# Kernel optimization log

Measured on AMD Instinct MI355X. Metric: run time of the kernel, lower is better.

The kernel has to match this reference:

```python
import jax, jax.numpy as jnp
import numpy as np

DIM = 128
HEADS = 4
HEAD_DIM = DIM // HEADS
SCALE = HEAD_DIM ** -0.5


def setup_inputs() -> dict:
    k0 = jax.random.key(0)
    ks = jax.random.split(k0, 20)
    B, N, Hq, Wq_, Hk, Wk_ = 1, 6, 100, 100, 16, 44
    s = 0.02
    return {
        "query": jax.random.normal(ks[0], (B, DIM, Hq, Wq_), jnp.float32),
        "key": jax.random.normal(ks[1], (B, N, DIM, Hk, Wk_), jnp.float32),
        "value": jax.random.normal(ks[2], (B, N, DIM, Hk, Wk_), jnp.float32),
        "depth": jax.random.uniform(ks[3], (B, N, 1, Hk, Wk_), jnp.float32),
        "depth_confidence": jax.random.uniform(ks[4], (B, N, 1, Hk, Wk_), jnp.float32),
        "skip": jax.random.normal(ks[5], (B, DIM, Hq, Wq_), jnp.float32),
        "Wq": jax.random.normal(ks[6], (DIM, DIM), jnp.float32) * s,
        "bq": jnp.zeros((DIM,), jnp.float32),
        "Wk": jax.random.normal(ks[7], (DIM, DIM), jnp.float32) * s,
        "bk": jnp.zeros((DIM,), jnp.float32),
        "Wv": jax.random.normal(ks[8], (DIM, DIM), jnp.float32) * s,
        "bv": jnp.zeros((DIM,), jnp.float32),
        "Wo": jax.random.normal(ks[9], (DIM, DIM), jnp.float32) * s,
        "bo": jnp.zeros((DIM,), jnp.float32),
        "dw1": jax.random.normal(ks[10], (DIM // 4, 1), jnp.float32) * s,  # 1x1 conv: 1 -> dim/4
        "db1": jnp.zeros((DIM // 4,), jnp.float32),
        "dw2": jax.random.normal(ks[11], (HEADS, DIM // 4), jnp.float32) * s,  # 1x1 conv: dim/4 -> heads
        "db2": jnp.zeros((HEADS,), jnp.float32),
    }


def _forward(query, key, value, depth, depth_confidence, skip,
             Wq, bq, Wk, bk, Wv, bv, Wo, bo, dw1, db1, dw2, db2):
    B, dim, Hq, Wq_ = query.shape
    N, Hk, Wk_ = key.shape[1], key.shape[3], key.shape[4]
    Lq, Lk = Hq * Wq_, N * Hk * Wk_

    # b d h w -> b (h w) d
    qf = jnp.transpose(query, (0, 2, 3, 1)).reshape(B, Lq, dim)
    # b n d h w -> b (n h w) d
    kf = jnp.transpose(key, (0, 1, 3, 4, 2)).reshape(B, Lk, dim)
    vf = jnp.transpose(value, (0, 1, 3, 4, 2)).reshape(B, Lk, dim)

    def heads(x, W, b):  # (B,L,dim) -> (B,H,L,hd)
        y = x @ W.T + b
        return jnp.transpose(y.reshape(B, -1, HEADS, HEAD_DIM), (0, 2, 1, 3))

    Q = heads(qf, Wq, bq)
    K = heads(kf, Wk, bk)
    V = heads(vf, Wv, bv)

    attn = jnp.einsum('bhqd,bhkd->bhqk', Q, K) * SCALE  # (B,H,Lq,Lk)

    # depth weighting bias: two 1x1 convs + softmax over heads channel
    d = jnp.transpose(depth, (0, 1, 3, 4, 2))  # (B,N,Hk,Wk,1)
    t = jax.nn.relu(d @ dw1.T + db1)            # (B,N,Hk,Wk,dim/4)
    t = t @ dw2.T + db2                          # (B,N,Hk,Wk,heads)
    dw = jax.nn.softmax(t, axis=-1)
    conf = jnp.transpose(depth_confidence, (0, 1, 3, 4, 2))  # (B,N,Hk,Wk,1)
    cw = conf * dw                               # (B,N,Hk,Wk,heads)
    bias = 0.1 * jnp.transpose(cw, (0, 4, 1, 2, 3)).reshape(B, HEADS, 1, Lk)

    attn = jax.nn.softmax(attn + bias, axis=-1)
    out = jnp.einsum('bhqk,bhkd->bhqd', attn, V)             # (B,H,Lq,hd)
    out = jnp.transpose(out, (0, 2, 1, 3)).reshape(B, Lq, dim)
    out = out @ Wo.T + bo
    out = jnp.transpose(out.reshape(B, Hq, Wq_, dim), (0, 3, 1, 2))
    return out + skip


def reference(query, key, value, depth, depth_confidence, skip,
              Wq, bq, Wk, bk, Wv, bv, Wo, bo, dw1, db1, dw2, db2):
    return _forward(query, key, value, depth, depth_confidence, skip,
                    Wq, bq, Wk, bk, Wv, bv, Wo, bo, dw1, db1, dw2, db2)
```

## Files before the change

### kernel.cpp

```cpp
#include <hip/hip_runtime.h>
#include <stdint.h>

#define LQ 10000
#define LK 4224
#define NQB 313
#define SCALE 0.17677669529663687f
#define LOG2E 1.44269504088896341f
#define SCALE2 (SCALE * LOG2E)

typedef __bf16 bf16x8 __attribute__((ext_vector_type(8)));
typedef __bf16 bf16x4 __attribute__((ext_vector_type(4)));
typedef float  f32x4  __attribute__((ext_vector_type(4)));
typedef unsigned short u16x4 __attribute__((ext_vector_type(4)));

__device__ __forceinline__ unsigned short f2b(float f) {
  union { float f; unsigned u; } v; v.f = f;
  unsigned r = v.u + 0x7fffu + ((v.u >> 16) & 1u);
  return (unsigned short)(r >> 16);
}

__global__ void misc_kernel(
    const float* __restrict__ depth, const float* __restrict__ conf,
    const float* __restrict__ dw1, const float* __restrict__ db1,
    const float* __restrict__ dw2, const float* __restrict__ db2,
    const float* __restrict__ Wq, const float* __restrict__ Wk,
    const float* __restrict__ Wv, const float* __restrict__ Wo,
    float* __restrict__ biasArr,
    unsigned short* __restrict__ Wqb, unsigned short* __restrict__ Wkb,
    unsigned short* __restrict__ Wvb, unsigned short* __restrict__ Wob) {
  int b = blockIdx.x, t = threadIdx.x;
  if (b < 256) {
    int i = b * 256 + t;
    int m = i >> 14, j = i & 16383;
    const float* src = (m == 0) ? Wq : (m == 1) ? Wk : (m == 2) ? Wv : Wo;
    unsigned short* dst = (m == 0) ? Wqb : (m == 1) ? Wkb : (m == 2) ? Wvb : Wob;
    dst[j] = f2b(src[j]);
    return;
  }
  int k = (b - 256) * 256 + t;
  if (k >= LK) return;
  float d = depth[k], c = conf[k];
  float t2[4];
#pragma unroll
  for (int hh = 0; hh < 4; ++hh) t2[hh] = db2[hh];
  for (int cc = 0; cc < 32; ++cc) {
    float t1 = fmaxf(fmaf(d, dw1[cc], db1[cc]), 0.f);
#pragma unroll
    for (int hh = 0; hh < 4; ++hh) t2[hh] = fmaf(t1, dw2[hh * 32 + cc], t2[hh]);
  }
  float mx = fmaxf(fmaxf(t2[0], t2[1]), fmaxf(t2[2], t2[3]));
  float e[4], s = 0.f;
#pragma unroll
  for (int hh = 0; hh < 4; ++hh) { e[hh] = __expf(t2[hh] - mx); s += e[hh]; }
  float f = 0.1f * c / s * LOG2E;
#pragma unroll
  for (int hh = 0; hh < 4; ++hh) biasArr[hh * LK + k] = f * e[hh];
}

__global__ __launch_bounds__(256) void proj_q_kernel(
    const float* __restrict__ X, const unsigned short* __restrict__ Wb,
    const float* __restrict__ bias, unsigned short* __restrict__ Y) {
  __shared__ __align__(16) unsigned short Xb[64][136];
  int t = threadIdx.x;
  int l0 = blockIdx.x * 64;
#pragma unroll
  for (int i = 0; i < 32; ++i) {
    int e = t + 256 * i;
    int d = e >> 6, c = e & 63;
    int l = l0 + c;
    Xb[c][d] = f2b(l < LQ ? X[(size_t)d * LQ + l] : 0.f);
  }
  __syncthreads();
  int wv = t >> 6, lane = t & 63, lm = lane & 15, lg = lane >> 4;
  const f32x4 zf = {0.f, 0.f, 0.f, 0.f};
  bf16x8 af[4];
#pragma unroll
  for (int kk = 0; kk < 4; ++kk)
    af[kk] = *(const bf16x8*)&Xb[wv * 16 + lm][kk * 32 + lg * 8];
  f32x4 acc[8] = {zf, zf, zf, zf, zf, zf, zf, zf};
#pragma unroll
  for (int kk = 0; kk < 4; ++kk)
#pragma unroll
    for (int ni = 0; ni < 8; ++ni) {
      bf16x8 bfr = *(const bf16x8*)(Wb + (size_t)(ni * 16 + lm) * 128 + kk * 32 + lg * 8);
      acc[ni] = __builtin_amdgcn_mfma_f32_16x16x32_bf16(af[kk], bfr, acc[ni], 0, 0, 0);
    }
#pragma unroll
  for (int ni = 0; ni < 8; ++ni)
#pragma unroll
    for (int r = 0; r < 4; ++r) {
      int l = l0 + wv * 16 + lg * 4 + r;
      int dout = ni * 16 + lm;
      Y[(size_t)l * 128 + dout] = f2b((acc[ni][r] + bias[dout]) * SCALE2);
    }
}

__global__ __launch_bounds__(256) void proj_kv_kernel(
    const float* __restrict__ key, const float* __restrict__ value,
    const unsigned short* __restrict__ Wkb, const float* __restrict__ bk,
    const unsigned short* __restrict__ Wvb, const float* __restrict__ bv,
    unsigned short* __restrict__ Kb, unsigned short* __restrict__ Vt) {
  __shared__ __align__(16) unsigned short Xb[64][136];
  int t = threadIdx.x;
  int isV = blockIdx.y;
  const float* X = isV ? value : key;
  const unsigned short* Wb = isV ? Wvb : Wkb;
  const float* bb = isV ? bv : bk;
  int k0 = blockIdx.x * 64;
  int n = k0 / 704, p0 = k0 % 704;
  const float* Xn = X + (size_t)n * 128 * 704 + p0;
#pragma unroll
  for (int i = 0; i < 32; ++i) {
    int e = t + 256 * i;
    int d = e >> 6, c = e & 63;
    Xb[c][d] = f2b(Xn[(size_t)d * 704 + c]);
  }
  __syncthreads();
  int wv = t >> 6, lane = t & 63, lm = lane & 15, lg = lane >> 4;
  const f32x4 zf = {0.f, 0.f, 0.f, 0.f};
  bf16x8 af[4];
#pragma unroll
  for (int kk = 0; kk < 4; ++kk)
    af[kk] = *(const bf16x8*)&Xb[wv * 16 + lm][kk * 32 + lg * 8];
  f32x4 acc[8] = {zf, zf, zf, zf, zf, zf, zf, zf};
#pragma unroll
  for (int kk = 0; kk < 4; ++kk)
#pragma unroll
    for (int ni = 0; ni < 8; ++ni) {
      bf16x8 bfr = *(const bf16x8*)(Wb + (size_t)(ni * 16 + lm) * 128 + kk * 32 + lg * 8);
      acc[ni] = __builtin_amdgcn_mfma_f32_16x16x32_bf16(af[kk], bfr, acc[ni], 0, 0, 0);
    }
  if (!isV) {
#pragma unroll
    for (int ni = 0; ni < 8; ++ni)
#pragma unroll
      for (int r = 0; r < 4; ++r) {
        int k = k0 + wv * 16 + lg * 4 + r;
        int dout = ni * 16 + lm;
        Kb[(size_t)k * 128 + dout] = f2b(acc[ni][r] + bb[dout]);
      }
  } else {
#pragma unroll
    for (int ni = 0; ni < 8; ++ni)
#pragma unroll
      for (int r = 0; r < 4; ++r) {
        int k = k0 + wv * 16 + lg * 4 + r;
        int dout = ni * 16 + lm;
        Vt[(size_t)dout * LK + k] = f2b(acc[ni][r] + bb[dout]);
      }
  }
}

__global__ __launch_bounds__(256) void attn_part_kernel(
    const unsigned short* __restrict__ Qb, const unsigned short* __restrict__ Kb,
    const unsigned short* __restrict__ Vt, const float* __restrict__ biasArr,
    float* __restrict__ Opart, float* __restrict__ Ml, int tpc, int C) {
  __shared__ __align__(16) unsigned short P_lds[4][32][64];
  int t = threadIdx.x;
  int wv = t >> 6;
  int qb = blockIdx.x * 4 + wv;
  if (qb >= NQB) return;
  int h = blockIdx.y, c = blockIdx.z;
  int lane = t & 63, lm = lane & 15, lg = lane >> 4;
  const f32x4 zf = {0.f, 0.f, 0.f, 0.f};

  bf16x8 qf[2];
#pragma unroll
  for (int mi = 0; mi < 2; ++mi)
    qf[mi] = *(const bf16x8*)(Qb + (size_t)(qb * 32 + mi * 16 + lm) * 128 + h * 32 + lg * 8);

  f32x4 acc[2][2] = {{zf, zf}, {zf, zf}};
  float mrun[2] = {-1e30f, -1e30f}, lrun[2] = {0.f, 0.f};

  const float* bias_h = biasArr + h * LK;
  const unsigned short* Kh = Kb + h * 32;
  const unsigned short* Vh = Vt + (size_t)h * 32 * LK;

  int wr_half = (lg & 1) * 4;
  int swz = lm & 7;

  int kb_end = c * tpc + tpc;
  for (int kb = c * tpc; kb < kb_end; ++kb) {
    int k0 = kb * 64;
    bf16x8 kf[4];
#pragma unroll
    for (int ni = 0; ni < 4; ++ni)
      kf[ni] = *(const bf16x8*)(Kh + (size_t)(k0 + ni * 16 + lm) * 128 + lg * 8);
    f32x4 bvv[4];
#pragma unroll
    for (int ni = 0; ni < 4; ++ni)
      bvv[ni] = *(const f32x4*)(bias_h + k0 + ni * 16 + lg * 4);
    f32x4 S[2][4];
#pragma unroll
    for (int mi = 0; mi < 2; ++mi)
#pragma unroll
      for (int ni = 0; ni < 4; ++ni)
        S[mi][ni] = __builtin_amdgcn_mfma_f32_16x16x32_bf16(kf[ni], qf[mi], bvv[ni], 0, 0, 0);

#pragma unroll
    for (int mi = 0; mi < 2; ++mi) {
      float pmax = -1e30f;
#pragma unroll
      for (int ni = 0; ni < 4; ++ni)
#pragma unroll
        for (int r = 0; r < 4; ++r)
          pmax = fmaxf(pmax, S[mi][ni][r]);
      pmax = fmaxf(pmax, __shfl_xor(pmax, 16));
      pmax = fmaxf(pmax, __shfl_xor(pmax, 32));
      float mn = fmaxf(mrun[mi], pmax);
      float fac = exp2f(mrun[mi] - mn);
      mrun[mi] = mn;
      float psum = 0.f;
#pragma unroll
      for (int ni = 0; ni < 4; ++ni) {
        bf16x4 pk;
#pragma unroll
        for (int r = 0; r < 4; ++r) {
          float p = exp2f(S[mi][ni][r] - mn);
          psum += p;
          pk[r] = (__bf16)p;
        }
        int chunk = (2 * ni + (lg >> 1)) ^ swz;
        *(bf16x4*)&P_lds[wv][mi * 16 + lm][chunk * 8 + wr_half] = pk;
      }
      psum += __shfl_xor(psum, 16);
      psum += __shfl_xor(psum, 32);
      lrun[mi] = fmaf(lrun[mi], fac, psum);
      float fac_t[4];
#pragma unroll
      for (int r = 0; r < 4; ++r) fac_t[r] = __shfl(fac, lg * 4 + r);
#pragma unroll
      for (int nd = 0; nd < 2; ++nd)
#pragma unroll
        for (int r = 0; r < 4; ++r) acc[mi][nd][r] *= fac_t[r];
    }
    asm volatile("" ::: "memory");
    __builtin_amdgcn_sched_barrier(0);
    bf16x8 pa[2][2], vfr[2][2];
#pragma unroll
    for (int mi = 0; mi < 2; ++mi)
#pragma unroll
      for (int kk = 0; kk < 2; ++kk) {
        int chunk = (4 * kk + lg) ^ swz;
        pa[mi][kk] = *(const bf16x8*)&P_lds[wv][mi * 16 + lm][chunk * 8];
      }
#pragma unroll
    for (int kk = 0; kk < 2; ++kk)
#pragma unroll
      for (int nd = 0; nd < 2; ++nd)
        vfr[kk][nd] = *(const bf16x8*)(Vh + (size_t)(nd * 16 + lm) * LK + k0 + kk * 32 + lg * 8);
#pragma unroll
    for (int mi = 0; mi < 2; ++mi)
#pragma unroll
      for (int nd = 0; nd < 2; ++nd)
#pragma unroll
        for (int kk = 0; kk < 2; ++kk)
          acc[mi][nd] = __builtin_amdgcn_mfma_f32_16x16x32_bf16(pa[mi][kk], vfr[kk][nd], acc[mi][nd], 0, 0, 0);
    asm volatile("" ::: "memory");
    __builtin_amdgcn_sched_barrier(0);
  }
  size_t pbase = (size_t)(qb * 4 + h) * C + c;
  float* Op = Opart + pbase * 1024;
#pragma unroll
  for (int mi = 0; mi < 2; ++mi)
#pragma unroll
    for (int nd = 0; nd < 2; ++nd)
#pragma unroll
      for (int r = 0; r < 4; ++r)
        Op[(mi * 16 + lg * 4 + r) * 32 + nd * 16 + lm] = acc[mi][nd][r];
  if (lane < 16) {
    float* MlB = Ml + pbase * 64;
#pragma unroll
    for (int mi = 0; mi < 2; ++mi) {
      MlB[mi * 16 + lm] = mrun[mi];
      MlB[32 + mi * 16 + lm] = lrun[mi];
    }
  }
}

__global__ __launch_bounds__(256) void combine_kernel(
    const float* __restrict__ Opart, const float* __restrict__ Ml,
    unsigned short* __restrict__ Ob, int C) {
  __shared__ float wls[4][7][32];
  int t = threadIdx.x, wv = t >> 6, lane = t & 63;
  int qb = blockIdx.x * 4 + wv;
  if (qb >= NQB) return;
  int h = blockIdx.y;
  size_t base = (size_t)(qb * 4 + h) * C;
  if (lane < 32) {
    float M = -1e30f;
    for (int c = 0; c < C; ++c)
      M = fmaxf(M, Ml[(base + c) * 64 + lane]);
    float lt = 0.f;
    for (int c = 0; c < C; ++c) {
      float w = exp2f(Ml[(base + c) * 64 + lane] - M);
      wls[wv][c][lane] = w;
      lt += Ml[(base + c) * 64 + 32 + lane] * w;
    }
    wls[wv][6][lane] = 1.f / lt;
  }
  asm volatile("" ::: "memory");
  __builtin_amdgcn_sched_barrier(0);
  const float* Op = Opart + base * 1024;
#pragma unroll
  for (int j = 0; j < 4; ++j) {
    int q = j * 8 + (lane >> 3);
    int d = (lane & 7) * 4;
    f32x4 accv = {0.f, 0.f, 0.f, 0.f};
    for (int c = 0; c < C; ++c) {
      f32x4 v = *(const f32x4*)(Op + c * 1024 + j * 256 + lane * 4);
      float w = wls[wv][c][q];
#pragma unroll
      for (int i = 0; i < 4; ++i) accv[i] = fmaf(v[i], w, accv[i]);
    }
    float linv = wls[wv][6][q];
    u16x4 o4;
#pragma unroll
    for (int i = 0; i < 4; ++i) o4[i] = f2b(accv[i] * linv);
    *(u16x4*)(Ob + (size_t)(qb * 32 + q) * 128 + h * 32 + d) = o4;
  }
}

__global__ __launch_bounds__(256) void epi_kernel(
    const unsigned short* __restrict__ Ob, const unsigned short* __restrict__ Wob,
    const float* __restrict__ bo, const float* __restrict__ skip,
    float* __restrict__ out) {
  int t = threadIdx.x, wv = t >> 6, lane = t & 63, lm = lane & 15, lg = lane >> 4;
  int l0 = blockIdx.x * 64;
  const f32x4 zf = {0.f, 0.f, 0.f, 0.f};
  bf16x8 af[2][4];
#pragma unroll
  for (int mi = 0; mi < 2; ++mi)
#pragma unroll
    for (int kk = 0; kk < 4; ++kk)
      af[mi][kk] = *(const bf16x8*)(Wob + (size_t)(wv * 32 + mi * 16 + lm) * 128 + kk * 32 + lg * 8);
  f32x4 acc[2][4] = {{zf, zf, zf, zf}, {zf, zf, zf, zf}};
#pragma unroll
  for (int kk = 0; kk < 4; ++kk) {
    bf16x8 bfr[4];
#pragma unroll
    for (int ni = 0; ni < 4; ++ni)
      bfr[ni] = *(const bf16x8*)(Ob + (size_t)(l0 + ni * 16 + lm) * 128 + kk * 32 + lg * 8);
#pragma unroll
    for (int mi = 0; mi < 2; ++mi)
#pragma unroll
      for (int ni = 0; ni < 4; ++ni)
        acc[mi][ni] = __builtin_amdgcn_mfma_f32_16x16x32_bf16(af[mi][kk], bfr[ni], acc[mi][ni], 0, 0, 0);
  }
#pragma unroll
  for (int mi = 0; mi < 2; ++mi)
#pragma unroll
    for (int r = 0; r < 4; ++r) {
      int dout = wv * 32 + mi * 16 + lg * 4 + r;
      float bb = bo[dout];
#pragma unroll
      for (int ni = 0; ni < 4; ++ni) {
        int l = l0 + ni * 16 + lm;
        if (l < LQ)
          out[(size_t)dout * LQ + l] = acc[mi][ni][r] + bb + skip[(size_t)dout * LQ + l];
      }
    }
}

extern "C" void kernel_launch(void* const* d_in, const int* in_sizes, int n_in,
                              void* d_out, int out_size, void* d_ws, size_t ws_size,
                              hipStream_t stream) {
  const float* query = (const float*)d_in[0];
  const float* key   = (const float*)d_in[1];
  const float* value = (const float*)d_in[2];
  const float* depth = (const float*)d_in[3];
  const float* conf  = (const float*)d_in[4];
  const float* skip  = (const float*)d_in[5];
  const float* Wq = (const float*)d_in[6];   const float* bq = (const float*)d_in[7];
  const float* Wk = (const float*)d_in[8];   const float* bk = (const float*)d_in[9];
  const float* Wv = (const float*)d_in[10];  const float* bv = (const float*)d_in[11];
  const float* Wo = (const float*)d_in[12];  const float* bo = (const float*)d_in[13];
  const float* dw1 = (const float*)d_in[14]; const float* db1 = (const float*)d_in[15];
  const float* dw2 = (const float*)d_in[16]; const float* db2 = (const float*)d_in[17];
  float* out = (float*)d_out;
  char* ws = (char*)d_ws;

  unsigned short* Qb   = (unsigned short*)(ws + 0);
  unsigned short* Kb   = (unsigned short*)(ws + 2572288);
  unsigned short* Vt   = (unsigned short*)(ws + 3653632);
  float*          bias = (float*)        (ws + 4734976);
  unsigned short* Wqb  = (unsigned short*)(ws + 4802560);
  unsigned short* Wkb  = (unsigned short*)(ws + 4835328);
  unsigned short* Wvb  = (unsigned short*)(ws + 4868096);
  unsigned short* Wob  = (unsigned short*)(ws + 4900864);
  unsigned short* Ob   = (unsigned short*)(ws + 4933632);
  const size_t splitOff = 7505920;

  int C = 1;
  {
    const int cand[4] = {6, 3, 2, 1};
    for (int i = 0; i < 4; ++i) {
      size_t need = splitOff + (size_t)NQB * 4 * cand[i] * (4096 + 256);
      if (ws_size >= need) { C = cand[i]; break; }
    }
  }
  int tpc = 66 / C;
  float* Opart = (float*)(ws + splitOff);
  float* Ml    = (float*)(ws + splitOff + (size_t)NQB * 4 * C * 4096);

  hipLaunchKernelGGL(misc_kernel, dim3(273), dim3(256), 0, stream,
                     depth, conf, dw1, db1, dw2, db2, Wq, Wk, Wv, Wo,
                     bias, Wqb, Wkb, Wvb, Wob);
  hipLaunchKernelGGL(proj_q_kernel, dim3(157), dim3(256), 0, stream,
                     query, Wqb, bq, Qb);
  hipLaunchKernelGGL(proj_kv_kernel, dim3(66, 2), dim3(256), 0, stream,
                     key, value, Wkb, bk, Wvb, bv, Kb, Vt);
  hipLaunchKernelGGL(attn_part_kernel, dim3(79, 4, C), dim3(256), 0, stream,
                     Qb, Kb, Vt, bias, Opart, Ml, tpc, C);
  hipLaunchKernelGGL(combine_kernel, dim3(79, 4), dim3(256), 0, stream,
                     Opart, Ml, Ob, C);
  hipLaunchKernelGGL(epi_kernel, dim3(157), dim3(256), 0, stream,
                     Ob, Wob, bo, skip, out);
}
```

Baseline: 260.5 us.

## Merge Q/K/V projections into one launch and fuse split-combine into epilogue

```diff
diff --git a/kernel.cpp b/kernel.cpp
--- a/kernel.cpp
+++ b/kernel.cpp
@@ -57,18 +57,45 @@
   for (int hh = 0; hh < 4; ++hh) biasArr[hh * LK + k] = f * e[hh];
 }
 
-__global__ __launch_bounds__(256) void proj_q_kernel(
-    const float* __restrict__ X, const unsigned short* __restrict__ Wb,
-    const float* __restrict__ bias, unsigned short* __restrict__ Y) {
+__global__ __launch_bounds__(256) void proj_kernel(
+    const float* __restrict__ query, const float* __restrict__ key,
+    const float* __restrict__ value,
+    const unsigned short* __restrict__ Wqb, const float* __restrict__ bq,
+    const unsigned short* __restrict__ Wkb, const float* __restrict__ bk,
+    const unsigned short* __restrict__ Wvb, const float* __restrict__ bv,
+    unsigned short* __restrict__ Qb, unsigned short* __restrict__ Kb,
+    unsigned short* __restrict__ Vt) {
   __shared__ __align__(16) unsigned short Xb[64][136];
   int t = threadIdx.x;
-  int l0 = blockIdx.x * 64;
-#pragma unroll
-  for (int i = 0; i < 32; ++i) {
-    int e = t + 256 * i;
-    int d = e >> 6, c = e & 63;
-    int l = l0 + c;
-    Xb[c][d] = f2b(l < LQ ? X[(size_t)d * LQ + l] : 0.f);
+  int bid = blockIdx.x;
+  int isQ = (bid < 157);
+  int kvid = bid - 157;
+  int isV = (kvid >= 66);
+  if (isV) kvid -= 66;
+
+  const unsigned short* Wb = isQ ? Wqb : (isV ? Wvb : Wkb);
+  const float* bb = isQ ? bq : (isV ? bv : bk);
+
+  if (isQ) {
+    int l0 = bid * 64;
+#pragma unroll
+    for (int i = 0; i < 32; ++i) {
+      int e = t + 256 * i;
+      int d = e >> 6, c = e & 63;
+      int l = l0 + c;
+      Xb[c][d] = f2b(l < LQ ? query[(size_t)d * LQ + l] : 0.f);
+    }
+  } else {
+    const float* X = isV ? value : key;
+    int k0 = kvid * 64;
+    int n = k0 / 704, p0 = k0 % 704;
+    const float* Xn = X + (size_t)n * 128 * 704 + p0;
+#pragma unroll
+    for (int i = 0; i < 32; ++i) {
+      int e = t + 256 * i;
+      int d = e >> 6, c = e & 63;
+      Xb[c][d] = f2b(Xn[(size_t)d * 704 + c]);
+    }
   }
   __syncthreads();
   int wv = t >> 6, lane = t & 63, lm = lane & 15, lg = lane >> 4;
@@ -85,52 +112,18 @@
       bf16x8 bfr = *(const bf16x8*)(Wb + (size_t)(ni * 16 + lm) * 128 + kk * 32 + lg * 8);
       acc[ni] = __builtin_amdgcn_mfma_f32_16x16x32_bf16(af[kk], bfr, acc[ni], 0, 0, 0);
     }
-#pragma unroll
-  for (int ni = 0; ni < 8; ++ni)
-#pragma unroll
-    for (int r = 0; r < 4; ++r) {
-      int l = l0 + wv * 16 + lg * 4 + r;
-      int dout = ni * 16 + lm;
-      Y[(size_t)l * 128 + dout] = f2b((acc[ni][r] + bias[dout]) * SCALE2);
-    }
-}
-
-__global__ __launch_bounds__(256) void proj_kv_kernel(
-    const float* __restrict__ key, const float* __restrict__ value,
-    const unsigned short* __restrict__ Wkb, const float* __restrict__ bk,
-    const unsigned short* __restrict__ Wvb, const float* __restrict__ bv,
-    unsigned short* __restrict__ Kb, unsigned short* __restrict__ Vt) {
-  __shared__ __align__(16) unsigned short Xb[64][136];
-  int t = threadIdx.x;
-  int isV = blockIdx.y;
-  const float* X = isV ? value : key;
-  const unsigned short* Wb = isV ? Wvb : Wkb;
-  const float* bb = isV ? bv : bk;
-  int k0 = blockIdx.x * 64;
-  int n = k0 / 704, p0 = k0 % 704;
-  const float* Xn = X + (size_t)n * 128 * 704 + p0;
-#pragma unroll
-  for (int i = 0; i < 32; ++i) {
-    int e = t + 256 * i;
-    int d = e >> 6, c = e & 63;
-    Xb[c][d] = f2b(Xn[(size_t)d * 704 + c]);
-  }
-  __syncthreads();
-  int wv = t >> 6, lane = t & 63, lm = lane & 15, lg = lane >> 4;
-  const f32x4 zf = {0.f, 0.f, 0.f, 0.f};
-  bf16x8 af[4];
-#pragma unroll
-  for (int kk = 0; kk < 4; ++kk)
-    af[kk] = *(const bf16x8*)&Xb[wv * 16 + lm][kk * 32 + lg * 8];
-  f32x4 acc[8] = {zf, zf, zf, zf, zf, zf, zf, zf};
-#pragma unroll
-  for (int kk = 0; kk < 4; ++kk)
-#pragma unroll
-    for (int ni = 0; ni < 8; ++ni) {
-      bf16x8 bfr = *(const bf16x8*)(Wb + (size_t)(ni * 16 + lm) * 128 + kk * 32 + lg * 8);
-      acc[ni] = __builtin_amdgcn_mfma_f32_16x16x32_bf16(af[kk], bfr, acc[ni], 0, 0, 0);
-    }
-  if (!isV) {
+  if (isQ) {
+    int l0 = bid * 64;
+#pragma unroll
+    for (int ni = 0; ni < 8; ++ni)
+#pragma unroll
+      for (int r = 0; r < 4; ++r) {
+        int l = l0 + wv * 16 + lg * 4 + r;
+        int dout = ni * 16 + lm;
+        Qb[(size_t)l * 128 + dout] = f2b((acc[ni][r] + bb[dout]) * SCALE2);
+      }
+  } else if (!isV) {
+    int k0 = kvid * 64;
 #pragma unroll
     for (int ni = 0; ni < 8; ++ni)
 #pragma unroll
@@ -140,6 +133,7 @@
         Kb[(size_t)k * 128 + dout] = f2b(acc[ni][r] + bb[dout]);
       }
   } else {
+    int k0 = kvid * 64;
 #pragma unroll
     for (int ni = 0; ni < 8; ++ni)
 #pragma unroll
@@ -186,16 +180,16 @@
 #pragma unroll
     for (int ni = 0; ni < 4; ++ni)
       kf[ni] = *(const bf16x8*)(Kh + (size_t)(k0 + ni * 16 + lm) * 128 + lg * 8);
+    f32x4 S[2][4];
+#pragma unroll
+    for (int mi = 0; mi < 2; ++mi)
+#pragma unroll
+      for (int ni = 0; ni < 4; ++ni)
+        S[mi][ni] = __builtin_amdgcn_mfma_f32_16x16x32_bf16(kf[ni], qf[mi], zf, 0, 0, 0);
     f32x4 bvv[4];
 #pragma unroll
     for (int ni = 0; ni < 4; ++ni)
       bvv[ni] = *(const f32x4*)(bias_h + k0 + ni * 16 + lg * 4);
-    f32x4 S[2][4];
-#pragma unroll
-    for (int mi = 0; mi < 2; ++mi)
-#pragma unroll
-      for (int ni = 0; ni < 4; ++ni)
-        S[mi][ni] = __builtin_amdgcn_mfma_f32_16x16x32_bf16(kf[ni], qf[mi], bvv[ni], 0, 0, 0);
 
 #pragma unroll
     for (int mi = 0; mi < 2; ++mi) {
@@ -203,8 +197,11 @@
 #pragma unroll
       for (int ni = 0; ni < 4; ++ni)
 #pragma unroll
-        for (int r = 0; r < 4; ++r)
-          pmax = fmaxf(pmax, S[mi][ni][r]);
+        for (int r = 0; r < 4; ++r) {
+          float x = S[mi][ni][r] + bvv[ni][r];
+          S[mi][ni][r] = x;
+          pmax = fmaxf(pmax, x);
+        }
       pmax = fmaxf(pmax, __shfl_xor(pmax, 16));
       pmax = fmaxf(pmax, __shfl_xor(pmax, 32));
       float mn = fmaxf(mrun[mi], pmax);
@@ -278,55 +275,66 @@
   }
 }
 
-__global__ __launch_bounds__(256) void combine_kernel(
+__global__ __launch_bounds__(256) void epi_kernel(
     const float* __restrict__ Opart, const float* __restrict__ Ml,
-    unsigned short* __restrict__ Ob, int C) {
+    const unsigned short* __restrict__ Wob, const float* __restrict__ bo,
+    const float* __restrict__ skip, float* __restrict__ out, int C) {
+  __shared__ __align__(16) unsigned short ObT[64][136];
   __shared__ float wls[4][7][32];
   int t = threadIdx.x, wv = t >> 6, lane = t & 63;
-  int qb = blockIdx.x * 4 + wv;
-  if (qb >= NQB) return;
-  int h = blockIdx.y;
-  size_t base = (size_t)(qb * 4 + h) * C;
-  if (lane < 32) {
-    float M = -1e30f;
-    for (int c = 0; c < C; ++c)
-      M = fmaxf(M, Ml[(base + c) * 64 + lane]);
-    float lt = 0.f;
-    for (int c = 0; c < C; ++c) {
-      float w = exp2f(Ml[(base + c) * 64 + lane] - M);
-      wls[wv][c][lane] = w;
-      lt += Ml[(base + c) * 64 + 32 + lane] * w;
-    }
-    wls[wv][6][lane] = 1.f / lt;
-  }
-  asm volatile("" ::: "memory");
-  __builtin_amdgcn_sched_barrier(0);
-  const float* Op = Opart + base * 1024;
-#pragma unroll
-  for (int j = 0; j < 4; ++j) {
-    int q = j * 8 + (lane >> 3);
-    int d = (lane & 7) * 4;
-    f32x4 accv = {0.f, 0.f, 0.f, 0.f};
-    for (int c = 0; c < C; ++c) {
-      f32x4 v = *(const f32x4*)(Op + c * 1024 + j * 256 + lane * 4);
-      float w = wls[wv][c][q];
-#pragma unroll
-      for (int i = 0; i < 4; ++i) accv[i] = fmaf(v[i], w, accv[i]);
-    }
-    float linv = wls[wv][6][q];
-    u16x4 o4;
-#pragma unroll
-    for (int i = 0; i < 4; ++i) o4[i] = f2b(accv[i] * linv);
-    *(u16x4*)(Ob + (size_t)(qb * 32 + q) * 128 + h * 32 + d) = o4;
-  }
-}
-
-__global__ __launch_bounds__(256) void epi_kernel(
-    const unsigned short* __restrict__ Ob, const unsigned short* __restrict__ Wob,
-    const float* __restrict__ bo, const float* __restrict__ skip,
-    float* __restrict__ out) {
-  int t = threadIdx.x, wv = t >> 6, lane = t & 63, lm = lane & 15, lg = lane >> 4;
-  int l0 = blockIdx.x * 64;
+  int bx = blockIdx.x, l0 = bx * 64;
+  int h = wv;
+
+#pragma unroll
+  for (int s = 0; s < 2; ++s) {
+    int qb = bx * 2 + s;
+    if (qb < NQB) {
+      size_t base = (size_t)(qb * 4 + h) * C;
+      if (lane < 32) {
+        float M = -1e30f;
+        for (int c = 0; c < C; ++c)
+          M = fmaxf(M, Ml[(base + c) * 64 + lane]);
+        float lt = 0.f;
+        for (int c = 0; c < C; ++c) {
+          float w = exp2f(Ml[(base + c) * 64 + lane] - M);
+          wls[wv][c][lane] = w;
+          lt += Ml[(base + c) * 64 + 32 + lane] * w;
+        }
+        wls[wv][6][lane] = 1.f / lt;
+      }
+      asm volatile("" ::: "memory");
+      __builtin_amdgcn_sched_barrier(0);
+      const float* Op = Opart + base * 1024;
+#pragma unroll
+      for (int j = 0; j < 4; ++j) {
+        int q = j * 8 + (lane >> 3);
+        int d = (lane & 7) * 4;
+        f32x4 accv = {0.f, 0.f, 0.f, 0.f};
+        for (int c = 0; c < C; ++c) {
+          f32x4 v = *(const f32x4*)(Op + c * 1024 + j * 256 + lane * 4);
+          float w = wls[wv][c][q];
+#pragma unroll
+          for (int i = 0; i < 4; ++i) accv[i] = fmaf(v[i], w, accv[i]);
+        }
+        float linv = wls[wv][6][q];
+        u16x4 o4;
+#pragma unroll
+        for (int i = 0; i < 4; ++i) o4[i] = f2b(accv[i] * linv);
+        *(u16x4*)&ObT[s * 32 + q][h * 32 + d] = o4;
+      }
+    } else {
+#pragma unroll
+      for (int j = 0; j < 4; ++j) {
+        int q = j * 8 + (lane >> 3);
+        int d = (lane & 7) * 4;
+        u16x4 z = {0, 0, 0, 0};
+        *(u16x4*)&ObT[s * 32 + q][h * 32 + d] = z;
+      }
+    }
+  }
+  __syncthreads();
+
+  int lm = lane & 15, lg = lane >> 4;
   const f32x4 zf = {0.f, 0.f, 0.f, 0.f};
   bf16x8 af[2][4];
 #pragma unroll
@@ -340,7 +348,7 @@
     bf16x8 bfr[4];
 #pragma unroll
     for (int ni = 0; ni < 4; ++ni)
-      bfr[ni] = *(const bf16x8*)(Ob + (size_t)(l0 + ni * 16 + lm) * 128 + kk * 32 + lg * 8);
+      bfr[ni] = *(const bf16x8*)&ObT[ni * 16 + lm][kk * 32 + lg * 8];
 #pragma unroll
     for (int mi = 0; mi < 2; ++mi)
 #pragma unroll
@@ -388,7 +396,6 @@
   unsigned short* Wkb  = (unsigned short*)(ws + 4835328);
   unsigned short* Wvb  = (unsigned short*)(ws + 4868096);
   unsigned short* Wob  = (unsigned short*)(ws + 4900864);
-  unsigned short* Ob   = (unsigned short*)(ws + 4933632);
   const size_t splitOff = 7505920;
 
   int C = 1;
@@ -406,14 +413,10 @@
   hipLaunchKernelGGL(misc_kernel, dim3(273), dim3(256), 0, stream,
                      depth, conf, dw1, db1, dw2, db2, Wq, Wk, Wv, Wo,
                      bias, Wqb, Wkb, Wvb, Wob);
-  hipLaunchKernelGGL(proj_q_kernel, dim3(157), dim3(256), 0, stream,
-                     query, Wqb, bq, Qb);
-  hipLaunchKernelGGL(proj_kv_kernel, dim3(66, 2), dim3(256), 0, stream,
-                     key, value, Wkb, bk, Wvb, bv, Kb, Vt);
+  hipLaunchKernelGGL(proj_kernel, dim3(289), dim3(256), 0, stream,
+                     query, key, value, Wqb, bq, Wkb, bk, Wvb, bv, Qb, Kb, Vt);
   hipLaunchKernelGGL(attn_part_kernel, dim3(79, 4, C), dim3(256), 0, stream,
                      Qb, Kb, Vt, bias, Opart, Ml, tpc, C);
-  hipLaunchKernelGGL(combine_kernel, dim3(79, 4), dim3(256), 0, stream,
-                     Opart, Ml, Ob, C);
   hipLaunchKernelGGL(epi_kernel, dim3(157), dim3(256), 0, stream,
-                     Ob, Wob, bo, skip, out);
-}
+                     Opart, Ml, Wob, bo, skip, out, C);
+}
```

New measurement: 249.1 us. 4.4% less time.
